# Kernel optimization log

Measured on AMD Instinct MI355X. Metric: run time of the kernel, lower is better.

The kernel has to match this reference:

```python
import jax, jax.numpy as jnp
import numpy as np
import math

B, S, DIM = 2, 2048, 2048
H, KV = 32, 8
HD = DIM // H          # 64
REP = H // KV          # 4
NEG = -1e9


def setup_inputs() -> dict:
    key = jax.random.key(0)
    ks = jax.random.split(key, 8)
    x = jax.random.normal(ks[0], (B, S, DIM), dtype=jnp.float32)
    # RoPE frequencies: theta = 10000^{-2i/d}, angles = pos * theta
    inv_freq = 1.0 / (10000.0 ** (jnp.arange(0, HD, 2, dtype=jnp.float32) / HD))  # [HD/2]
    angles = jnp.arange(S, dtype=jnp.float32)[:, None] * inv_freq[None, :]        # [S, HD/2]
    freqs_cos = jnp.cos(angles)
    freqs_sin = jnp.sin(angles)
    # additive causal mask [1,1,S,S]
    causal = jnp.tril(jnp.ones((S, S), dtype=bool))
    mask = jnp.where(causal, 0.0, NEG).astype(jnp.float32)[None, None]
    sc = 1.0 / math.sqrt(DIM)
    wq = jax.random.normal(ks[1], (DIM, H * HD), dtype=jnp.float32) * sc
    wk = jax.random.normal(ks[2], (DIM, KV * HD), dtype=jnp.float32) * sc
    wv = jax.random.normal(ks[3], (DIM, KV * HD), dtype=jnp.float32) * sc
    wo = jax.random.normal(ks[4], (H * HD, DIM), dtype=jnp.float32) * sc
    return {"x": x, "freqs_cos": freqs_cos, "freqs_sin": freqs_sin,
            "mask": mask, "wq": wq, "wk": wk, "wv": wv, "wo": wo}


def _rope(t, cos, sin):
    # t: [B,S,nh,HD]; interleaved (even, odd) pairs == view_as_complex layout
    te, to = t[..., 0::2], t[..., 1::2]
    c = cos[None, :, None, :]  # [1,S,1,HD/2]
    s = sin[None, :, None, :]
    oe = te * c - to * s
    oo = te * s + to * c
    return jnp.stack([oe, oo], axis=-1).reshape(t.shape)


def reference(x, freqs_cos, freqs_sin, mask, wq, wk, wv, wo):
    b, s, _ = x.shape
    q = (x @ wq).reshape(b, s, H, HD)
    k = (x @ wk).reshape(b, s, KV, HD)
    v = (x @ wv).reshape(b, s, KV, HD)
    q = _rope(q, freqs_cos, freqs_sin)
    k = _rope(k, freqs_cos, freqs_sin)
    # GQA without materializing repeat_interleave: group q heads by kv head
    # repeat_interleave maps query head h -> kv head h // REP
    qg = q.transpose(0, 2, 1, 3).reshape(b, KV, REP, s, HD)  # [B,KV,REP,S,HD]
    kg = k.transpose(0, 2, 1, 3)                              # [B,KV,S,HD]
    vg = v.transpose(0, 2, 1, 3)
    scores = jnp.einsum('bgrqd,bgkd->bgrqk', qg, kg) / math.sqrt(HD)
    scores = scores + mask[:, :, None]                        # [1,1,1,S,S] broadcast
    attn = jax.nn.softmax(scores, axis=-1)
    out = jnp.einsum('bgrqk,bgkd->bgrqd', attn, vg)           # [B,KV,REP,S,HD]
    out = out.reshape(b, H, s, HD).transpose(0, 2, 1, 3).reshape(b, s, H * HD)
    return out @ wo
```

## Files before the change

kernel.cpp:

```cpp
#include <hip/hip_runtime.h>
#include <hip/hip_bf16.h>

#define B_ 2
#define S_ 2048
#define DIM_ 2048
#define H_ 32
#define KV_ 8
#define HD_ 64

typedef __bf16 bf16x8 __attribute__((ext_vector_type(8)));
typedef __bf16 bf16x4 __attribute__((ext_vector_type(4)));
typedef float f32x4 __attribute__((ext_vector_type(4)));
typedef float f32x16 __attribute__((ext_vector_type(16)));
typedef unsigned u32x2 __attribute__((ext_vector_type(2)));

#define GLOAD16(gp, lp) __builtin_amdgcn_global_load_lds( \
    (const __attribute__((address_space(1))) void*)(gp),  \
    (__attribute__((address_space(3))) void*)(lp), 16, 0, 0)

__global__ __launch_bounds__(256) void cast_f32_bf16_v4(const float* __restrict__ in,
                                                        __bf16* __restrict__ out, int n4) {
    int i = blockIdx.x * 256 + threadIdx.x;
    if (i >= n4) return;
    float4 v = ((const float4*)in)[i];
    bf16x4 o;
    o[0] = (__bf16)v.x; o[1] = (__bf16)v.y; o[2] = (__bf16)v.z; o[3] = (__bf16)v.w;
    ((bf16x4*)out)[i] = o;
}

__global__ __launch_bounds__(256) void transpose_all_t(const float* __restrict__ wq,
                                                       const float* __restrict__ wk,
                                                       const float* __restrict__ wv,
                                                       const float* __restrict__ wo,
                                                       __bf16* __restrict__ wqkv_t,
                                                       __bf16* __restrict__ wo_t) {
    __shared__ float t[32][33];
    const int bk = blockIdx.x * 32, bn = blockIdx.y * 32;
    const int tx = threadIdx.x & 31, ty = threadIdx.x >> 5;
    const float* W; __bf16* Wt; int N, src;
    if (blockIdx.z == 0) {
        Wt = wqkv_t;
        if (bn < 2048)      { W = wq; N = 2048; src = bn; }
        else if (bn < 2560) { W = wk; N = 512;  src = bn - 2048; }
        else                { W = wv; N = 512;  src = bn - 2560; }
    } else {
        if (bn >= 2048) return;
        Wt = wo_t; W = wo; N = 2048; src = bn;
    }
#pragma unroll
    for (int i = 0; i < 4; i++)
        t[ty * 4 + i][tx] = W[(size_t)(bk + ty * 4 + i) * N + src + tx];
    __syncthreads();
#pragma unroll
    for (int i = 0; i < 4; i++)
        Wt[(size_t)(bn + ty * 4 + i) * 2048 + bk + tx] = (__bf16)t[tx][ty * 4 + i];
}

__global__ __launch_bounds__(256) void rope_ip(__bf16* __restrict__ T,
                                               const float* __restrict__ cosb,
                                               const float* __restrict__ sinb,
                                               int nh, int total) {
    int idx = blockIdx.x * 256 + threadIdx.x;
    if (idx >= total) return;
    int npair = nh * 32;
    int r = idx / npair;
    int c = idx - r * npair;
    int hh = c >> 5, i = c & 31;
    int s = r & (S_ - 1);
    float cv = cosb[s * 32 + i], sv = sinb[s * 32 + i];
    __bf16* p = T + (size_t)r * (nh * HD_) + hh * HD_ + 2 * i;
    float e = (float)p[0], o = (float)p[1];
    p[0] = (__bf16)(e * cv - o * sv);
    p[1] = (__bf16)(e * sv + o * cv);
}

__global__ __launch_bounds__(256) void transpose_v_t(const __bf16* __restrict__ V,
                                                     __bf16* __restrict__ Vt) {
    __shared__ __bf16 t[32][33];
    const int bs = blockIdx.x * 32, bd = blockIdx.y * 32, bg = blockIdx.z;
    const int b = bg >> 3, g = bg & 7;
    const int tx = threadIdx.x & 31, ty = threadIdx.x >> 5;
#pragma unroll
    for (int i = 0; i < 4; i++)
        t[ty * 4 + i][tx] = V[(size_t)(b * S_ + bs + ty * 4 + i) * (KV_ * HD_) + g * HD_ + bd + tx];
    __syncthreads();
#pragma unroll
    for (int i = 0; i < 4; i++)
        Vt[(size_t)(bg * HD_ + bd + ty * 4 + i) * S_ + bs + tx] = t[tx][ty * 4 + i];
}

__global__ __launch_bounds__(256)
void gemm_bt(const __bf16* __restrict__ A, const __bf16* __restrict__ Bt,
             void* __restrict__ C0, void* __restrict__ C1, void* __restrict__ C2,
             int M, int N, int K, int n0, int n1, int out_f32) {
    __shared__ __align__(16) __bf16 lA[128 * 32];
    __shared__ __align__(16) __bf16 lB[128 * 32];
    const int tid = threadIdx.x;
    const int lane = tid & 63;
    const int wid = tid >> 6;
    const long i0 = (long)blockIdx.x * 128;
    const long j0 = (long)blockIdx.y * 128;
    const int wr = (wid >> 1) * 64;
    const int wc = (wid & 1) * 64;
    const int sr = tid >> 2;
    const int sc = (tid & 3) * 8;
    const int fr = lane & 15;
    const int fg = lane >> 4;

    f32x4 acc[4][4] = {};

    const __bf16* Arow0 = A + (i0 + sr) * K + sc;
    const __bf16* Arow1 = A + (i0 + 64 + sr) * K + sc;
    const __bf16* Brow0 = Bt + (j0 + sr) * K + sc;
    const __bf16* Brow1 = Bt + (j0 + 64 + sr) * K + sc;
    __bf16* ldA0 = lA + tid * 8;
    __bf16* ldA1 = lA + 2048 + tid * 8;
    __bf16* ldB0 = lB + tid * 8;
    __bf16* ldB1 = lB + 2048 + tid * 8;

    for (int k0 = 0; k0 < K; k0 += 32) {
        __syncthreads();
        GLOAD16(Arow0 + k0, ldA0);
        GLOAD16(Arow1 + k0, ldA1);
        GLOAD16(Brow0 + k0, ldB0);
        GLOAD16(Brow1 + k0, ldB1);
        __syncthreads();
        bf16x8 af[4], bfr[4];
#pragma unroll
        for (int m = 0; m < 4; m++) af[m]  = *(bf16x8*)&lA[(wr + m * 16 + fr) * 32 + fg * 8];
#pragma unroll
        for (int n = 0; n < 4; n++) bfr[n] = *(bf16x8*)&lB[(wc + n * 16 + fr) * 32 + fg * 8];
#pragma unroll
        for (int m = 0; m < 4; m++)
#pragma unroll
            for (int n = 0; n < 4; n++)
                acc[m][n] = __builtin_amdgcn_mfma_f32_16x16x32_bf16(af[m], bfr[n], acc[m][n], 0, 0, 0);
    }

    void* base; long stride, cofs;
    if (j0 < n0)           { base = C0; stride = n0;           cofs = 0; }
    else if (j0 < n0 + n1) { base = C1; stride = n1;           cofs = n0; }
    else                   { base = C2; stride = N - n0 - n1;  cofs = n0 + n1; }
#pragma unroll
    for (int m = 0; m < 4; m++)
#pragma unroll
        for (int n = 0; n < 4; n++)
#pragma unroll
            for (int j = 0; j < 4; j++) {
                long row = i0 + wr + m * 16 + fg * 4 + j;
                long col = j0 + wc + n * 16 + fr - cofs;
                float v = acc[m][n][j];
                if (out_f32) ((float*)base)[row * stride + col] = v;
                else         ((__bf16*)base)[row * stride + col] = (__bf16)v;
            }
}

__global__ __launch_bounds__(512, 2)
void gemm256(const __bf16* __restrict__ A, const __bf16* __restrict__ Bt,
             void* __restrict__ C0, void* __restrict__ C1, void* __restrict__ C2,
             int M, int N, int K, int n0, int n1, int out_f32) {
    __shared__ __align__(16) char smem[131072];
    char* lA = smem;
    char* lB = smem + 65536;
    const int tid = threadIdx.x, lane = tid & 63, wid = tid >> 6;
    const int wr2 = wid >> 2, wc2 = wid & 3;
    const int fr = lane & 15, fg = lane >> 4;
    const long i0 = (long)blockIdx.x * 256;
    const long j0 = (long)blockIdx.y * 256;

    const int r0 = tid >> 3;
    const int cc = ((tid & 7) ^ (r0 & 7)) * 8;
    const __bf16* pA = A + (i0 + r0) * (long)K + cc;
    const __bf16* pB = Bt + (j0 + r0) * (long)K + cc;
    const int NT = K >> 6;

    f32x4 acc[8][4] = {};

#define STGA(h, kt, buf) do { \
    GLOAD16(pA + (long)((h) * 128) * K + (kt) * 64,      lA + (buf) * 32768 + (h) * 16384 + tid * 16); \
    GLOAD16(pA + (long)((h) * 128 + 64) * K + (kt) * 64, lA + (buf) * 32768 + (h) * 16384 + 8192 + tid * 16); } while (0)
#define STGB(h, kt, buf) do { \
    GLOAD16(pB + (long)((h) * 128) * K + (kt) * 64,      lB + (buf) * 32768 + (h) * 16384 + tid * 16); \
    GLOAD16(pB + (long)((h) * 128 + 64) * K + (kt) * 64, lB + (buf) * 32768 + (h) * 16384 + 8192 + tid * 16); } while (0)

    STGA(0, 0, 0); STGB(0, 0, 0); STGB(1, 0, 0); STGA(1, 0, 0);

    for (int kt = 0; kt < NT; ++kt) {
        const int cur = kt & 1, nxt = cur ^ 1;
        const bool nl = (kt + 1 < NT);
        const char* cA = lA + cur * 32768;
        const char* cB = lB + cur * 32768;
        bf16x8 af[4], bfv[4];

        auto rdA = [&](int mf, int ks) -> bf16x8 {
            int row = wr2 * 128 + mf * 16 + fr;
            return *(const bf16x8*)(cA + row * 128 + (((ks << 2) | fg) ^ (row & 7)) * 16);
        };
        auto rdB = [&](int nf, int ks) -> bf16x8 {
            int row = wc2 * 64 + nf * 16 + fr;
            return *(const bf16x8*)(cB + row * 128 + (((ks << 2) | fg) ^ (row & 7)) * 16);
        };

        if (nl) { STGA(0, kt + 1, nxt); STGB(0, kt + 1, nxt); }
        if (nl) asm volatile("s_waitcnt vmcnt(4)" ::: "memory");
        else    asm volatile("s_waitcnt vmcnt(0)" ::: "memory");
        __builtin_amdgcn_s_barrier();
        asm volatile("" ::: "memory");
#pragma unroll
        for (int nf = 0; nf < 4; nf++) bfv[nf] = rdB(nf, 0);
#pragma unroll
        for (int mf = 0; mf < 4; mf++) af[mf] = rdA(mf, 0);
        __builtin_amdgcn_s_setprio(1);
#pragma unroll
        for (int mf = 0; mf < 4; mf++)
#pragma unroll
            for (int nf = 0; nf < 4; nf++)
                acc[mf][nf] = __builtin_amdgcn_mfma_f32_16x16x32_bf16(af[mf], bfv[nf], acc[mf][nf], 0, 0, 0);
        __builtin_amdgcn_s_setprio(0);
        __builtin_amdgcn_s_barrier();

#pragma unroll
        for (int mf = 0; mf < 4; mf++) af[mf] = rdA(4 + mf, 0);
        if (nl) { STGB(1, kt + 1, nxt); STGA(1, kt + 1, nxt); }
        __builtin_amdgcn_s_barrier();
        __builtin_amdgcn_s_setprio(1);
#pragma unroll
        for (int mf = 0; mf < 4; mf++)
#pragma unroll
            for (int nf = 0; nf < 4; nf++)
                acc[4 + mf][nf] = __builtin_amdgcn_mfma_f32_16x16x32_bf16(af[mf], bfv[nf], acc[4 + mf][nf], 0, 0, 0);
        __builtin_amdgcn_s_setprio(0);
        __builtin_amdgcn_s_barrier();

#pragma unroll
        for (int nf = 0; nf < 4; nf++) bfv[nf] = rdB(nf, 1);
#pragma unroll
        for (int mf = 0; mf < 4; mf++) af[mf] = rdA(mf, 1);
        __builtin_amdgcn_s_barrier();
        __builtin_amdgcn_s_setprio(1);
#pragma unroll
        for (int mf = 0; mf < 4; mf++)
#pragma unroll
            for (int nf = 0; nf < 4; nf++)
                acc[mf][nf] = __builtin_amdgcn_mfma_f32_16x16x32_bf16(af[mf], bfv[nf], acc[mf][nf], 0, 0, 0);
        __builtin_amdgcn_s_setprio(0);
        __builtin_amdgcn_s_barrier();

#pragma unroll
        for (int mf = 0; mf < 4; mf++) af[mf] = rdA(4 + mf, 1);
        __builtin_amdgcn_s_barrier();
        __builtin_amdgcn_s_setprio(1);
#pragma unroll
        for (int mf = 0; mf < 4; mf++)
#pragma unroll
            for (int nf = 0; nf < 4; nf++)
                acc[4 + mf][nf] = __builtin_amdgcn_mfma_f32_16x16x32_bf16(af[mf], bfv[nf], acc[4 + mf][nf], 0, 0, 0);
        __builtin_amdgcn_s_setprio(0);
        __builtin_amdgcn_s_barrier();
    }

    void* base; long stride, cofs;
    if (j0 < n0)           { base = C0; stride = n0;           cofs = 0; }
    else if (j0 < n0 + n1) { base = C1; stride = n1;           cofs = n0; }
    else                   { base = C2; stride = N - n0 - n1;  cofs = n0 + n1; }
#pragma unroll
    for (int mf = 0; mf < 8; mf++)
#pragma unroll
        for (int nf = 0; nf < 4; nf++)
#pragma unroll
            for (int j = 0; j < 4; j++) {
                long row = i0 + wr2 * 128 + mf * 16 + fg * 4 + j;
                long col = j0 + wc2 * 64 + nf * 16 + fr - cofs;
                float v = acc[mf][nf][j];
                if (out_f32) ((float*)base)[row * stride + col] = v;
                else         ((__bf16*)base)[row * stride + col] = (__bf16)v;
            }
#undef STGA
#undef STGB
}

__global__ __launch_bounds__(256, 4)
void attn_fwd(const __bf16* __restrict__ Q, const __bf16* __restrict__ Kb,
              const __bf16* __restrict__ Vt, __bf16* __restrict__ O,
              const float* __restrict__ fc, const float* __restrict__ fs) {
    extern __shared__ __align__(16) char smem[];
    __bf16* lK  = (__bf16*)smem;
    __bf16* lVt = (__bf16*)(smem + 16384);

    const int tid = threadIdx.x;
    const int lane = tid & 63;
    const int wid = tid >> 6;
    const int ln = lane & 31;
    const int hi = lane >> 5;

    const int id = blockIdx.x;
    const int g = id & 7;
    const int r = id >> 3;
    const int chunk = 15 - (r >> 3);
    const int hb = r & 7;
    const int b = hb & 1;
    const int h = g * 4 + (hb >> 1);
    const int QS = H_ * HD_, KS = KV_ * HD_;
    const float K2 = 0.18033688011112042f;
    const float mK = 8.0f * K2;

    const __bf16* Kbse = Kb + (size_t)(b * S_) * KS + g * HD_;
    const __bf16* Vbse = Vt + (size_t)((b * KV_ + g) * HD_) * S_;

    bf16x8 onesf;
#pragma unroll
    for (int j = 0; j < 8; j++) onesf[j] = (__bf16)1.0f;

    const int c0 = tid, c1 = tid + 256;
    const int kr0 = c0 & 63, kd0 = c0 >> 6;
    const int kr1 = c1 & 63, kd1 = c1 >> 6;
    const __bf16* Ksrc0 = Kbse + (size_t)kr0 * KS + kd0 * 8;
    const __bf16* Ksrc1 = Kbse + (size_t)kr1 * KS + kd1 * 8;
    const __bf16* Vsrc0 = Vbse + (size_t)kr0 * S_ + kd0 * 8;
    const __bf16* Vsrc1 = Vbse + (size_t)kr1 * S_ + kd1 * 8;

    auto stage = [&](int t, int buf) {
        GLOAD16(Ksrc0 + (size_t)t * 64 * KS, lK + buf * 4096 + c0 * 8);
        GLOAD16(Ksrc1 + (size_t)t * 64 * KS, lK + buf * 4096 + c1 * 8);
        GLOAD16(Vsrc0 + t * 64,              lVt + buf * 4096 + c0 * 8);
        GLOAD16(Vsrc1 + t * 64,              lVt + buf * 4096 + c1 * 8);
    };

    const int q0w = chunk * 128 + wid * 32;
    const int qrow = q0w + ln;
    const int nt = 2 * chunk + 2;
    const int nkv_w = (q0w >> 6) + 1;

    const __bf16* Qb = Q + (size_t)(b * S_ + qrow) * QS + h * HD_;
    const float* cz = fc + (size_t)qrow * 32;
    const float* sz = fs + (size_t)qrow * 32;
    bf16x8 qf[4];
#pragma unroll
    for (int kk = 0; kk < 4; kk++) {
        bf16x8 raw = *(const bf16x8*)(Qb + kk * 16 + hi * 8);
#pragma unroll
        for (int p = 0; p < 4; p++) {
            const int i = kk * 8 + hi * 4 + p;
            float cv = cz[i], sv = sz[i];
            float e = (float)raw[2 * p], o = (float)raw[2 * p + 1];
            qf[kk][2 * p]     = (__bf16)(e * cv - o * sv);
            qf[kk][2 * p + 1] = (__bf16)(e * sv + o * cv);
        }
    }

    f32x16 o0 = {}, o1 = {}, o2 = {};

    stage(0, 0);
    __syncthreads();

    for (int t = 0; t < nt; t++) {
        if (t + 1 < nt) stage(t + 1, (t + 1) & 1);
        if (t < nkv_w) {
            const char* lKc = (const char*)(lK + (t & 1) * 4096);
            const char* lVc = (const char*)(lVt + (t & 1) * 4096);
            const int p0 = t * 64;

            f32x16 s0 = {}, s1 = {};
            __builtin_amdgcn_s_setprio(1);
#pragma unroll
            for (int kk = 0; kk < 4; kk++) {
                bf16x8 ka = *(const bf16x8*)(lKc + (kk * 2 + hi) * 1024 + ln * 16);
                s0 = __builtin_amdgcn_mfma_f32_32x32x16_bf16(ka, qf[kk], s0, 0, 0, 0);
            }
#pragma unroll
            for (int kk = 0; kk < 4; kk++) {
                bf16x8 ka = *(const bf16x8*)(lKc + (kk * 2 + hi) * 1024 + (32 + ln) * 16);
                s1 = __builtin_amdgcn_mfma_f32_32x32x16_bf16(ka, qf[kk], s1, 0, 0, 0);
            }
            __builtin_amdgcn_s_setprio(0);

            if (t == nkv_w - 1) {
#pragma unroll
                for (int rr = 0; rr < 16; rr++) {
                    int crow = (rr & 3) + 8 * (rr >> 2) + 4 * hi;
                    if (p0 + crow > qrow)      s0[rr] = -1e30f;
                    if (p0 + 32 + crow > qrow) s1[rr] = -1e30f;
                }
            }

#pragma unroll
            for (int rr = 0; rr < 16; rr++) {
                s0[rr] = exp2f(s0[rr] * K2 - mK);
                s1[rr] = exp2f(s1[rr] * K2 - mK);
            }

            __builtin_amdgcn_s_setprio(1);
#pragma unroll
            for (int c = 0; c < 2; c++) {
                const f32x16& pe = c ? s1 : s0;
                unsigned w[4][2];
#pragma unroll
                for (int gi = 0; gi < 4; gi++)
#pragma unroll
                    for (int p = 0; p < 2; p++) {
                        unsigned short lo = __builtin_bit_cast(unsigned short, (__bf16)pe[4 * gi + 2 * p]);
                        unsigned short hp = __builtin_bit_cast(unsigned short, (__bf16)pe[4 * gi + 2 * p + 1]);
                        w[gi][p] = (unsigned)lo | ((unsigned)hp << 16);
                    }
                unsigned pw0[4], pw1[4];
#pragma unroll
                for (int p = 0; p < 2; p++) {
                    u32x2 ra = __builtin_amdgcn_permlane32_swap(w[0][p], w[1][p], false, false);
                    pw0[p] = ra[0]; pw0[2 + p] = ra[1];
                    u32x2 rb = __builtin_amdgcn_permlane32_swap(w[2][p], w[3][p], false, false);
                    pw1[p] = rb[0]; pw1[2 + p] = rb[1];
                }
                bf16x8 pa0 = __builtin_bit_cast(bf16x8, *(uint4*)pw0);
                bf16x8 pa1 = __builtin_bit_cast(bf16x8, *(uint4*)pw1);
#pragma unroll
                for (int half = 0; half < 2; half++) {
                    const int ks = 2 * c + half;
                    bf16x8 pa = half ? pa1 : pa0;
                    bf16x8 va0 = *(const bf16x8*)(lVc + (ks * 2 + hi) * 1024 + ln * 16);
                    bf16x8 va1 = *(const bf16x8*)(lVc + (ks * 2 + hi) * 1024 + (32 + ln) * 16);
                    o0 = __builtin_amdgcn_mfma_f32_32x32x16_bf16(va0, pa, o0, 0, 0, 0);
                    o1 = __builtin_amdgcn_mfma_f32_32x32x16_bf16(va1, pa, o1, 0, 0, 0);
                    o2 = __builtin_amdgcn_mfma_f32_32x32x16_bf16(onesf, pa, o2, 0, 0, 0);
                }
            }
            __builtin_amdgcn_s_setprio(0);
        }
        __syncthreads();
    }

    const float inv = 1.0f / o2[0];
    __bf16* Oq = O + (size_t)(b * S_ + qrow) * QS + h * HD_;
#pragma unroll
    for (int db = 0; db < 2; db++) {
        const f32x16& oo = db ? o1 : o0;
#pragma unroll
        for (int gi = 0; gi < 4; gi++) {
            bf16x4 pk;
#pragma unroll
            for (int j = 0; j < 4; j++) pk[j] = (__bf16)(oo[4 * gi + j] * inv);
            *(bf16x4*)(Oq + db * 32 + 8 * gi + 4 * hi) = pk;
        }
    }
}

extern "C" void kernel_launch(void* const* d_in, const int* in_sizes, int n_in,
                              void* d_out, int out_size, void* d_ws, size_t ws_size,
                              hipStream_t stream) {
    const float* x  = (const float*)d_in[0];
    const float* fc = (const float*)d_in[1];
    const float* fs = (const float*)d_in[2];
    const float* wq = (const float*)d_in[4];
    const float* wk = (const float*)d_in[5];
    const float* wv = (const float*)d_in[6];
    const float* wo = (const float*)d_in[7];
    float* out = (float*)d_out;

    const size_t N0 = (size_t)B_ * S_ * DIM_;
    const size_t N1 = (size_t)B_ * S_ * H_ * HD_;
    const size_t N2 = (size_t)B_ * S_ * KV_ * HD_;
    const size_t N3 = (size_t)DIM_ * H_ * HD_;
    const size_t N4 = (size_t)DIM_ * KV_ * HD_;

    __bf16* x_bf = (__bf16*)d_ws;
    __bf16* q_bf = x_bf + N0;
    __bf16* k_bf = q_bf + N1;
    __bf16* v_bf = k_bf + N2;
    __bf16* vt_bf = v_bf + N2;
    __bf16* wqkv_t = vt_bf + N2;
    __bf16* wo_t = wqkv_t + N3 + 2 * N4;
    __bf16* ao_bf = x_bf;

    cast_f32_bf16_v4<<<dim3(N0 / 4 / 256), 256, 0, stream>>>(x, x_bf, (int)(N0 / 4));
    transpose_all_t<<<dim3(64, 96, 2), 256, 0, stream>>>(wq, wk, wv, wo, wqkv_t, wo_t);

    gemm256<<<dim3(16, 12), 512, 0, stream>>>(x_bf, wqkv_t, q_bf, k_bf, v_bf,
                                              B_ * S_, 3 * 1024, DIM_, H_ * HD_, KV_ * HD_, 0);

    rope_ip<<<dim3(N2 / 2 / 256), 256, 0, stream>>>(k_bf, fc, fs, KV_, (int)(N2 / 2));
    transpose_v_t<<<dim3(64, 2, 16), 256, 0, stream>>>(v_bf, vt_bf);

    attn_fwd<<<dim3(1024), 256, 32768, stream>>>(q_bf, k_bf, vt_bf, ao_bf, fc, fs);

    gemm_bt<<<dim3(32, 16), 256, 0, stream>>>(ao_bf, wo_t, out, out, out,
                                              B_ * S_, DIM_, DIM_, DIM_, 0, 1);
}
```

Before: 220.5 us.

## Fuse K RoPE and V transpose into QKV GEMM epilogue; new output-projection GEMM

The QKV GEMM epilogue now applies RoPE to K using a lane shuffle to fetch the paired element, and writes V directly in transposed layout. This removes the separate rope_ip and transpose_v_t kernels and their extra memory passes. The output projection moves from a simple 128x128, single-buffered GEMM to a double-buffered 128x256 tile kernel with swizzled LDS and setprio. The fused epilogue adds scattered cos/sin loads and strided Vt stores, and the new GEMM launches only 256 blocks.

```diff
diff --git a/kernel.cpp b/kernel.cpp
--- a/kernel.cpp
+++ b/kernel.cpp
@@ -56,112 +56,15 @@
         Wt[(size_t)(bn + ty * 4 + i) * 2048 + bk + tx] = (__bf16)t[tx][ty * 4 + i];
 }
 
-__global__ __launch_bounds__(256) void rope_ip(__bf16* __restrict__ T,
-                                               const float* __restrict__ cosb,
-                                               const float* __restrict__ sinb,
-                                               int nh, int total) {
-    int idx = blockIdx.x * 256 + threadIdx.x;
-    if (idx >= total) return;
-    int npair = nh * 32;
-    int r = idx / npair;
-    int c = idx - r * npair;
-    int hh = c >> 5, i = c & 31;
-    int s = r & (S_ - 1);
-    float cv = cosb[s * 32 + i], sv = sinb[s * 32 + i];
-    __bf16* p = T + (size_t)r * (nh * HD_) + hh * HD_ + 2 * i;
-    float e = (float)p[0], o = (float)p[1];
-    p[0] = (__bf16)(e * cv - o * sv);
-    p[1] = (__bf16)(e * sv + o * cv);
-}
-
-__global__ __launch_bounds__(256) void transpose_v_t(const __bf16* __restrict__ V,
-                                                     __bf16* __restrict__ Vt) {
-    __shared__ __bf16 t[32][33];
-    const int bs = blockIdx.x * 32, bd = blockIdx.y * 32, bg = blockIdx.z;
-    const int b = bg >> 3, g = bg & 7;
-    const int tx = threadIdx.x & 31, ty = threadIdx.x >> 5;
-#pragma unroll
-    for (int i = 0; i < 4; i++)
-        t[ty * 4 + i][tx] = V[(size_t)(b * S_ + bs + ty * 4 + i) * (KV_ * HD_) + g * HD_ + bd + tx];
-    __syncthreads();
-#pragma unroll
-    for (int i = 0; i < 4; i++)
-        Vt[(size_t)(bg * HD_ + bd + ty * 4 + i) * S_ + bs + tx] = t[tx][ty * 4 + i];
-}
-
-__global__ __launch_bounds__(256)
-void gemm_bt(const __bf16* __restrict__ A, const __bf16* __restrict__ Bt,
-             void* __restrict__ C0, void* __restrict__ C1, void* __restrict__ C2,
-             int M, int N, int K, int n0, int n1, int out_f32) {
-    __shared__ __align__(16) __bf16 lA[128 * 32];
-    __shared__ __align__(16) __bf16 lB[128 * 32];
-    const int tid = threadIdx.x;
-    const int lane = tid & 63;
-    const int wid = tid >> 6;
-    const long i0 = (long)blockIdx.x * 128;
-    const long j0 = (long)blockIdx.y * 128;
-    const int wr = (wid >> 1) * 64;
-    const int wc = (wid & 1) * 64;
-    const int sr = tid >> 2;
-    const int sc = (tid & 3) * 8;
-    const int fr = lane & 15;
-    const int fg = lane >> 4;
-
-    f32x4 acc[4][4] = {};
-
-    const __bf16* Arow0 = A + (i0 + sr) * K + sc;
-    const __bf16* Arow1 = A + (i0 + 64 + sr) * K + sc;
-    const __bf16* Brow0 = Bt + (j0 + sr) * K + sc;
-    const __bf16* Brow1 = Bt + (j0 + 64 + sr) * K + sc;
-    __bf16* ldA0 = lA + tid * 8;
-    __bf16* ldA1 = lA + 2048 + tid * 8;
-    __bf16* ldB0 = lB + tid * 8;
-    __bf16* ldB1 = lB + 2048 + tid * 8;
-
-    for (int k0 = 0; k0 < K; k0 += 32) {
-        __syncthreads();
-        GLOAD16(Arow0 + k0, ldA0);
-        GLOAD16(Arow1 + k0, ldA1);
-        GLOAD16(Brow0 + k0, ldB0);
-        GLOAD16(Brow1 + k0, ldB1);
-        __syncthreads();
-        bf16x8 af[4], bfr[4];
-#pragma unroll
-        for (int m = 0; m < 4; m++) af[m]  = *(bf16x8*)&lA[(wr + m * 16 + fr) * 32 + fg * 8];
-#pragma unroll
-        for (int n = 0; n < 4; n++) bfr[n] = *(bf16x8*)&lB[(wc + n * 16 + fr) * 32 + fg * 8];
-#pragma unroll
-        for (int m = 0; m < 4; m++)
-#pragma unroll
-            for (int n = 0; n < 4; n++)
-                acc[m][n] = __builtin_amdgcn_mfma_f32_16x16x32_bf16(af[m], bfr[n], acc[m][n], 0, 0, 0);
-    }
-
-    void* base; long stride, cofs;
-    if (j0 < n0)           { base = C0; stride = n0;           cofs = 0; }
-    else if (j0 < n0 + n1) { base = C1; stride = n1;           cofs = n0; }
-    else                   { base = C2; stride = N - n0 - n1;  cofs = n0 + n1; }
-#pragma unroll
-    for (int m = 0; m < 4; m++)
-#pragma unroll
-        for (int n = 0; n < 4; n++)
-#pragma unroll
-            for (int j = 0; j < 4; j++) {
-                long row = i0 + wr + m * 16 + fg * 4 + j;
-                long col = j0 + wc + n * 16 + fr - cofs;
-                float v = acc[m][n][j];
-                if (out_f32) ((float*)base)[row * stride + col] = v;
-                else         ((__bf16*)base)[row * stride + col] = (__bf16)v;
-            }
-}
-
 __global__ __launch_bounds__(512, 2)
-void gemm256(const __bf16* __restrict__ A, const __bf16* __restrict__ Bt,
-             void* __restrict__ C0, void* __restrict__ C1, void* __restrict__ C2,
-             int M, int N, int K, int n0, int n1, int out_f32) {
+void gemm256_qkv(const __bf16* __restrict__ A, const __bf16* __restrict__ Bt,
+                 __bf16* __restrict__ q_bf, __bf16* __restrict__ k_bf,
+                 __bf16* __restrict__ vt_bf,
+                 const float* __restrict__ fc, const float* __restrict__ fs) {
     __shared__ __align__(16) char smem[131072];
     char* lA = smem;
     char* lB = smem + 65536;
+    const int K = DIM_;
     const int tid = threadIdx.x, lane = tid & 63, wid = tid >> 6;
     const int wr2 = wid >> 2, wc2 = wid & 3;
     const int fr = lane & 15, fg = lane >> 4;
@@ -258,25 +161,134 @@
         __builtin_amdgcn_s_setprio(0);
         __builtin_amdgcn_s_barrier();
     }
-
-    void* base; long stride, cofs;
-    if (j0 < n0)           { base = C0; stride = n0;           cofs = 0; }
-    else if (j0 < n0 + n1) { base = C1; stride = n1;           cofs = n0; }
-    else                   { base = C2; stride = N - n0 - n1;  cofs = n0 + n1; }
-#pragma unroll
-    for (int mf = 0; mf < 8; mf++)
-#pragma unroll
-        for (int nf = 0; nf < 4; nf++)
-#pragma unroll
-            for (int j = 0; j < 4; j++) {
-                long row = i0 + wr2 * 128 + mf * 16 + fg * 4 + j;
-                long col = j0 + wc2 * 64 + nf * 16 + fr - cofs;
-                float v = acc[mf][nf][j];
-                if (out_f32) ((float*)base)[row * stride + col] = v;
-                else         ((__bf16*)base)[row * stride + col] = (__bf16)v;
-            }
 #undef STGA
 #undef STGB
+
+    const long col0 = j0 + wc2 * 64;
+    if (j0 < 2048) {
+#pragma unroll
+        for (int mf = 0; mf < 8; mf++)
+#pragma unroll
+            for (int nf = 0; nf < 4; nf++)
+#pragma unroll
+                for (int j = 0; j < 4; j++) {
+                    long row = i0 + wr2 * 128 + mf * 16 + fg * 4 + j;
+                    q_bf[row * 2048 + col0 + nf * 16 + fr] = (__bf16)acc[mf][nf][j];
+                }
+    } else if (j0 < 2560) {
+#pragma unroll
+        for (int mf = 0; mf < 8; mf++)
+#pragma unroll
+            for (int nf = 0; nf < 4; nf++) {
+                const int kd = (int)(col0 + nf * 16 + fr - 2048);
+                const int i_ = (kd & 63) >> 1;
+                const float sgn = (fr & 1) ? 1.0f : -1.0f;
+#pragma unroll
+                for (int j = 0; j < 4; j++) {
+                    long row = i0 + wr2 * 128 + mf * 16 + fg * 4 + j;
+                    int s = (int)(row & (S_ - 1));
+                    float cv = fc[s * 32 + i_], sv = fs[s * 32 + i_];
+                    float v = acc[mf][nf][j];
+                    float p = __shfl_xor(v, 1, 64);
+                    k_bf[row * 512 + kd] = (__bf16)(v * cv + sgn * sv * p);
+                }
+            }
+    } else {
+#pragma unroll
+        for (int mf = 0; mf < 8; mf++)
+#pragma unroll
+            for (int nf = 0; nf < 4; nf++) {
+                const int vd = (int)(col0 + nf * 16 + fr - 2560);
+                long row0 = i0 + wr2 * 128 + mf * 16 + fg * 4;
+                int b = (int)(row0 >> 11);
+                int s = (int)(row0 & (S_ - 1));
+                bf16x4 pk;
+#pragma unroll
+                for (int j = 0; j < 4; j++) pk[j] = (__bf16)acc[mf][nf][j];
+                *(bf16x4*)(vt_bf + ((size_t)(b * KV_ + (vd >> 6)) * HD_ + (vd & 63)) * S_ + s) = pk;
+            }
+    }
+}
+
+__global__ __launch_bounds__(512, 2)
+void gemm256_o(const __bf16* __restrict__ A, const __bf16* __restrict__ Bt,
+               float* __restrict__ C) {
+    __shared__ __align__(16) char smem[98304];
+    char* lA = smem;
+    char* lB = smem + 32768;
+    const int K = DIM_;
+    const int tid = threadIdx.x, lane = tid & 63, wid = tid >> 6;
+    const int wr2 = wid >> 2, wc2 = wid & 3;
+    const int fr = lane & 15, fg = lane >> 4;
+    const int id = blockIdx.x;
+    const long i0 = (long)(id >> 3) * 128;
+    const long j0 = (long)(id & 7) * 256;
+
+    const int r0 = tid >> 3;
+    const int cc = ((tid & 7) ^ (r0 & 7)) * 8;
+    const __bf16* pA = A + (i0 + r0) * (long)K + cc;
+    const __bf16* pB = Bt + (j0 + r0) * (long)K + cc;
+    const int NT = K >> 6;
+
+    f32x4 acc[4][4] = {};
+
+#define STG(kt, buf) do { \
+    GLOAD16(pA + (long)(kt) * 64,                  lA + (buf) * 16384 + tid * 16); \
+    GLOAD16(pA + (long)64 * K + (long)(kt) * 64,   lA + (buf) * 16384 + 8192 + tid * 16); \
+    GLOAD16(pB + (long)(kt) * 64,                  lB + (buf) * 32768 + tid * 16); \
+    GLOAD16(pB + (long)64 * K + (long)(kt) * 64,   lB + (buf) * 32768 + 8192 + tid * 16); \
+    GLOAD16(pB + (long)128 * K + (long)(kt) * 64,  lB + (buf) * 32768 + 16384 + tid * 16); \
+    GLOAD16(pB + (long)192 * K + (long)(kt) * 64,  lB + (buf) * 32768 + 24576 + tid * 16); } while (0)
+
+    STG(0, 0);
+
+    for (int kt = 0; kt < NT; ++kt) {
+        const int cur = kt & 1, nxt = cur ^ 1;
+        const bool nl = (kt + 1 < NT);
+        const char* cA = lA + cur * 16384;
+        const char* cB = lB + cur * 32768;
+
+        if (nl) STG(kt + 1, nxt);
+        if (nl) asm volatile("s_waitcnt vmcnt(6)" ::: "memory");
+        else    asm volatile("s_waitcnt vmcnt(0)" ::: "memory");
+        __builtin_amdgcn_s_barrier();
+        asm volatile("" ::: "memory");
+
+        bf16x8 af[4], bfv[4];
+#pragma unroll
+        for (int ks = 0; ks < 2; ks++) {
+#pragma unroll
+            for (int nf = 0; nf < 4; nf++) {
+                int row = wc2 * 64 + nf * 16 + fr;
+                bfv[nf] = *(const bf16x8*)(cB + row * 128 + (((ks << 2) | fg) ^ (row & 7)) * 16);
+            }
+#pragma unroll
+            for (int mf = 0; mf < 4; mf++) {
+                int row = wr2 * 64 + mf * 16 + fr;
+                af[mf] = *(const bf16x8*)(cA + row * 128 + (((ks << 2) | fg) ^ (row & 7)) * 16);
+            }
+            __builtin_amdgcn_s_setprio(1);
+#pragma unroll
+            for (int mf = 0; mf < 4; mf++)
+#pragma unroll
+                for (int nf = 0; nf < 4; nf++)
+                    acc[mf][nf] = __builtin_amdgcn_mfma_f32_16x16x32_bf16(af[mf], bfv[nf], acc[mf][nf], 0, 0, 0);
+            __builtin_amdgcn_s_setprio(0);
+        }
+        __builtin_amdgcn_s_barrier();
+    }
+#undef STG
+
+#pragma unroll
+    for (int mf = 0; mf < 4; mf++)
+#pragma unroll
+        for (int nf = 0; nf < 4; nf++)
+#pragma unroll
+            for (int j = 0; j < 4; j++) {
+                long row = i0 + wr2 * 64 + mf * 16 + fg * 4 + j;
+                long col = j0 + wc2 * 64 + nf * 16 + fr;
+                C[row * 2048 + col] = acc[mf][nf][j];
+            }
 }
 
 __global__ __launch_bounds__(256, 4)
@@ -464,8 +476,7 @@
     __bf16* x_bf = (__bf16*)d_ws;
     __bf16* q_bf = x_bf + N0;
     __bf16* k_bf = q_bf + N1;
-    __bf16* v_bf = k_bf + N2;
-    __bf16* vt_bf = v_bf + N2;
+    __bf16* vt_bf = k_bf + N2;
     __bf16* wqkv_t = vt_bf + N2;
     __bf16* wo_t = wqkv_t + N3 + 2 * N4;
     __bf16* ao_bf = x_bf;
@@ -473,14 +484,9 @@
     cast_f32_bf16_v4<<<dim3(N0 / 4 / 256), 256, 0, stream>>>(x, x_bf, (int)(N0 / 4));
     transpose_all_t<<<dim3(64, 96, 2), 256, 0, stream>>>(wq, wk, wv, wo, wqkv_t, wo_t);
 
-    gemm256<<<dim3(16, 12), 512, 0, stream>>>(x_bf, wqkv_t, q_bf, k_bf, v_bf,
-                                              B_ * S_, 3 * 1024, DIM_, H_ * HD_, KV_ * HD_, 0);
-
-    rope_ip<<<dim3(N2 / 2 / 256), 256, 0, stream>>>(k_bf, fc, fs, KV_, (int)(N2 / 2));
-    transpose_v_t<<<dim3(64, 2, 16), 256, 0, stream>>>(v_bf, vt_bf);
+    gemm256_qkv<<<dim3(16, 12), 512, 0, stream>>>(x_bf, wqkv_t, q_bf, k_bf, vt_bf, fc, fs);
 
     attn_fwd<<<dim3(1024), 256, 32768, stream>>>(q_bf, k_bf, vt_bf, ao_bf, fc, fs);
 
-    gemm_bt<<<dim3(32, 16), 256, 0, stream>>>(ao_bf, wo_t, out, out, out,
-                                              B_ * S_, DIM_, DIM_, DIM_, 0, 1);
-}
+    gemm256_o<<<dim3(256), 512, 0, stream>>>(ao_bf, wo_t, out);
+}
```

After: 197.2 us. -10.6%, faster.
